# Kernel optimization log

Hardware: AMD Instinct MI355X
Metric: run time of the kernel (lower is better)

## Reference

```python
import jax, jax.numpy as jnp
import numpy as np

N = 20000          # skill_num (nodes)
D = 128            # skill_embed_dim
E = 640000         # edges (avg degree 32)
T = 12             # seq_len
L = 3              # gcn_layers
PRESERVE = 0.1     # residual preserve_ratio


def setup_inputs() -> dict:
    key = jax.random.key(0)
    ks = jax.random.split(key, 8)
    demand_seq_emb = jax.random.normal(ks[0], (N, T, D), jnp.float32)
    supply_seq_emb = jax.random.normal(ks[1], (N, T, D), jnp.float32)
    edge_index = jax.random.randint(ks[2], (2, E), 0, N, dtype=jnp.int32)
    edge_attr = jax.random.uniform(ks[3], (E,), jnp.float32)
    emb_weight = jax.random.normal(ks[4], (N, D), jnp.float32) * 0.02
    fuse_W = jax.random.normal(ks[5], (D, 3 * D), jnp.float32) * (1.0 / np.sqrt(3 * D))
    fuse_b = jnp.zeros((D,), jnp.float32)
    gcn_W = jax.random.normal(ks[6], (L, D, D), jnp.float32) * (1.0 / np.sqrt(D))
    gcn_b = jnp.zeros((L, D), jnp.float32)
    return {
        "demand_seq_emb": demand_seq_emb,
        "supply_seq_emb": supply_seq_emb,
        "l": T, "t_s": 0, "t_e": T,                 # unused by forward (placeholders)
        "edge_index": edge_index,
        "edge_attr": edge_attr,
        "comm": 0, "skill_semantic_embed": 0, "init_emb": 0,  # unused placeholders
        "emb_weight": emb_weight,
        "fuse_W": fuse_W, "fuse_b": fuse_b,
        "gcn_W": gcn_W, "gcn_b": gcn_b,
    }


def _gcn_norm(src, dst, edge_w, n):
    """PyG gcn_norm with self-loops: norm_e = d^-1/2[src] * w_e * d^-1/2[dst]."""
    loop = jnp.arange(n, dtype=src.dtype)
    src2 = jnp.concatenate([src, loop])
    dst2 = jnp.concatenate([dst, loop])
    w2 = jnp.concatenate([edge_w, jnp.ones((n,), edge_w.dtype)])
    deg = jax.ops.segment_sum(w2, dst2, num_segments=n)
    dinv = jnp.where(deg > 0, jax.lax.rsqrt(deg), 0.0)
    norm = dinv[src2] * w2 * dinv[dst2]
    return src2, dst2, norm


def reference(demand_seq_emb, supply_seq_emb, l, t_s, t_e, edge_index, edge_attr,
              comm, skill_semantic_embed, init_emb,
              emb_weight, fuse_W, fuse_b, gcn_W, gcn_b):
    # fuse static embedding with last-step demand/supply sequence embeddings
    seq_last = jnp.concatenate([demand_seq_emb[:, -1, :], supply_seq_emb[:, -1, :]], axis=-1)  # [N,2D]
    fused = jnp.concatenate([emb_weight, seq_last], axis=-1) @ fuse_W.T + fuse_b  # [N,D]

    # edges are generated with all indices < skill_num, so the torch-side
    # `(edge_index < skill_num).all(0)` filter is the identity here.
    src, dst = edge_index[0], edge_index[1]
    src2, dst2, norm = _gcn_norm(src, dst, edge_attr, N)

    temp = fused
    for i in range(L):  # small fixed layer count
        x = temp @ gcn_W[i].T                                   # [N,D] linear (bias added post-agg)
        msg = norm[:, None] * x[src2]                           # gather + scale
        out = jax.ops.segment_sum(msg, dst2, num_segments=N) + gcn_b[i]  # scatter-add
        temp = (1.0 - PRESERVE) * out + PRESERVE * temp         # residual blend
    return temp  # skill_embs [N, D]
```

## Files before the change

### kernel.cpp

```cpp
#include <hip/hip_runtime.h>
#include <hip/hip_fp16.h>

#define NN 20000
#define DD 128
#define EE 640000
#define TSEQ 12
#define CAP 128
#define PADI 32

__device__ __forceinline__ void fma4(float4& acc, float a, const float4& w) {
  acc.x += a * w.x; acc.y += a * w.y; acc.z += a * w.z; acc.w += a * w.w;
}

__device__ __forceinline__ float4 h8_to_f4(uint2 v) {
  union { unsigned u; __half2 h; } a, b;
  a.u = v.x; b.u = v.y;
  float2 fa = __half22float2(a.h);
  float2 fb = __half22float2(b.h);
  return make_float4(fa.x, fa.y, fb.x, fb.y);
}

__device__ __forceinline__ uint2 f4_to_h8(float4 o) {
  union { unsigned u; __half2 h; } a, b;
  a.h = __floats2half2_rn(o.x, o.y);
  b.h = __floats2half2_rn(o.z, o.w);
  uint2 r; r.x = a.u; r.y = b.u;
  return r;
}

__global__ void k_prep(const float* __restrict__ fuse_W,
                       const float* __restrict__ gcn_W,
                       int* __restrict__ cnt_pad,
                       float* __restrict__ fuse_Wt,
                       float* __restrict__ gWt0,
                       __half* __restrict__ gWh) {
  int b = blockIdx.x;
  if (b < 625) {
    int i = b * 256 + threadIdx.x;
    ((int4*)cnt_pad)[i] = make_int4(0, 0, 0, 0);
  } else {
    int i = (b - 625) * 256 + threadIdx.x;
    if (i < 49152) {
      int k = i >> 7, d = i & 127;
      fuse_Wt[i] = fuse_W[d * 384 + k];
    } else if (i < 65536) {
      int j = i - 49152;
      int k = j >> 7, d = j & 127;
      gWt0[j] = gcn_W[d * 128 + k];
    } else if (i < 98304) {
      int j = i - 65536;
      int l = 1 + (j >> 14), jj = j & 16383;
      int k = jj >> 7, d = jj & 127;
      gWh[j] = (__half)gcn_W[l * 16384 + d * 128 + k];
    }
  }
}

#define G_TN 2
#define G_BN 32

template<int KC>
__device__ __forceinline__ void gemm_body(
    float* Ws, int gb,
    const float* a0, int s0, const float* a1, int s1, const float* a2, int s2,
    int nparts, const float* Wt, const float* bias, const float* deg,
    float* outf, uint2* outh)
{
  const int t = threadIdx.x;
  const int dq = t & 15;
  const int ng = t >> 4;
  const int n_base = gb * G_BN + ng * G_TN;

  float4 acc0[G_TN], acc1[G_TN];
  #pragma unroll
  for (int i = 0; i < G_TN; ++i) {
    acc0[i] = make_float4(0.f, 0.f, 0.f, 0.f);
    acc1[i] = make_float4(0.f, 0.f, 0.f, 0.f);
  }

  for (int p = 0; p < nparts; ++p) {
    const float* ap; int as;
    if (p == 0) { ap = a0; as = s0; }
    else if (p == 1) { ap = a1; as = s1; }
    else { ap = a2; as = s2; }
    const float* rp[G_TN];
    #pragma unroll
    for (int i = 0; i < G_TN; ++i) rp[i] = ap + (size_t)(n_base + i) * as;

    for (int c = 0; c < 128 / KC; ++c) {
      const float4* wsrc = (const float4*)(Wt + (p * 128 + c * KC) * 128);
      float4* wdst = (float4*)Ws;
      #pragma unroll
      for (int it = 0; it < KC / 8; ++it) wdst[it * 256 + t] = wsrc[it * 256 + t];
      __syncthreads();

      const int ks = c * KC;
      for (int k = 0; k < KC; k += 4) {
        float4 av[G_TN];
        #pragma unroll
        for (int i = 0; i < G_TN; ++i) av[i] = *(const float4*)(rp[i] + ks + k);
        #pragma unroll
        for (int j = 0; j < 4; ++j) {
          const float4 w0 = *(const float4*)&Ws[(k + j) * 128 + 4 * dq];
          const float4 w1 = *(const float4*)&Ws[(k + j) * 128 + 64 + 4 * dq];
          #pragma unroll
          for (int i = 0; i < G_TN; ++i) {
            float a = (j == 0) ? av[i].x : (j == 1) ? av[i].y : (j == 2) ? av[i].z : av[i].w;
            fma4(acc0[i], a, w0);
            fma4(acc1[i], a, w1);
          }
        }
      }
      __syncthreads();
    }
  }

  float4 b0 = make_float4(0.f,0.f,0.f,0.f), b1 = b0;
  if (bias) {
    b0 = *(const float4*)&bias[4 * dq];
    b1 = *(const float4*)&bias[64 + 4 * dq];
  }
  #pragma unroll
  for (int i = 0; i < G_TN; ++i) {
    int r = n_base + i;
    float4 o0 = make_float4(acc0[i].x + b0.x, acc0[i].y + b0.y,
                            acc0[i].z + b0.z, acc0[i].w + b0.w);
    float4 o1 = make_float4(acc1[i].x + b1.x, acc1[i].y + b1.y,
                            acc1[i].z + b1.z, acc1[i].w + b1.w);
    if (outf) {
      *(float4*)(outf + (size_t)r * DD + 4 * dq) = o0;
      *(float4*)(outf + (size_t)r * DD + 64 + 4 * dq) = o1;
    } else {
      float di = rsqrtf(deg[r]);
      o0.x *= di; o0.y *= di; o0.z *= di; o0.w *= di;
      o1.x *= di; o1.y *= di; o1.z *= di; o1.w *= di;
      outh[(size_t)r * 32 + dq] = f4_to_h8(o0);
      outh[(size_t)r * 32 + 16 + dq] = f4_to_h8(o1);
    }
  }
}

__global__ __launch_bounds__(256, 4) void k_mega(
    const float* __restrict__ emb, const float* __restrict__ demand,
    const float* __restrict__ supply,
    const float* __restrict__ fuse_Wt, const float* __restrict__ fuse_b,
    float* __restrict__ temp0,
    const int* __restrict__ src, const int* __restrict__ dst,
    const float* __restrict__ w,
    int* __restrict__ cnt_pad,
    uint2* __restrict__ csr)
{
  __shared__ float Ws[64 * 128];
  if (blockIdx.x < 625) {
    gemm_body<64>(Ws, blockIdx.x,
                  emb, 128, demand + 11 * 128, TSEQ * 128, supply + 11 * 128, TSEQ * 128,
                  3, fuse_Wt, fuse_b, nullptr, temp0, nullptr);
  } else {
    int e = (blockIdx.x - 625) * 256 + threadIdx.x;
    int s = src[e], d = dst[e];
    float we = w[e];
    int slot = atomicAdd(&cnt_pad[(size_t)d * PADI], 1);
    if (slot < CAP) csr[(size_t)d * CAP + slot] = make_uint2((unsigned)s, __float_as_uint(we));
  }
}

__global__ __launch_bounds__(256, 8) void k_deg(
    const int* __restrict__ cnt_pad, const uint2* __restrict__ csr,
    float* __restrict__ deg)
{
  const int t = threadIdx.x;
  const int lane = t & 7;
  const int ng = t >> 3;
  const int n = blockIdx.x * 32 + ng;
  int m = cnt_pad[(size_t)n * PADI]; if (m > CAP) m = CAP;
  const size_t base = (size_t)n * CAP;
  float s = 0.f;
  for (int j = lane; j < m; j += 8) s += __uint_as_float(csr[base + j].y);
  s += __shfl_xor(s, 1);
  s += __shfl_xor(s, 2);
  s += __shfl_xor(s, 4);
  if (lane == 0) deg[n] = 1.0f + s;
}

__global__ __launch_bounds__(256, 8) void k_gemm_x0(
    const float* __restrict__ temp0, const float* __restrict__ gWt0,
    const float* __restrict__ deg, uint2* __restrict__ outh)
{
  __shared__ float Ws[32 * 128];
  gemm_body<32>(Ws, blockIdx.x, temp0, 128, temp0, 128, temp0, 128,
                1, gWt0, nullptr, deg, nullptr, outh);
}

template<bool NEXT>
__global__ __launch_bounds__(256, 6) void k_agg_fused(
    const uint2* __restrict__ xh, const float* __restrict__ tin,
    const int* __restrict__ cnt_pad, const uint2* __restrict__ csr,
    const float* __restrict__ deg, const float* __restrict__ bias,
    const uint2* __restrict__ Wh,
    float* __restrict__ tout,
    uint2* __restrict__ xh_out)
{
  __shared__ float rows[NEXT ? 8 * 128 : 8];
  __shared__ uint2 Whs[NEXT ? 2048 : 8];

  const int t = threadIdx.x;
  const int dq = t & 31;
  const int nl = t >> 5;
  const int n = blockIdx.x * 8 + nl;

  if constexpr (NEXT) {
    #pragma unroll
    for (int i = 0; i < 8; ++i) Whs[i * 256 + t] = Wh[i * 256 + t];
  }

  const float di = rsqrtf(deg[n]);
  float4 acc = h8_to_f4(xh[(size_t)n * 32 + dq]);

  const size_t base = (size_t)n * CAP;
  int m = cnt_pad[(size_t)n * PADI]; if (m > CAP) m = CAP;
  int j = 0;
  for (; j + 16 <= m; j += 16) {
    uint2 c[16];
    #pragma unroll
    for (int u = 0; u < 16; ++u) c[u] = csr[base + j + u];
    uint2 v[16];
    #pragma unroll
    for (int u = 0; u < 16; ++u) v[u] = xh[(size_t)c[u].x * 32 + dq];
    #pragma unroll
    for (int u = 0; u < 16; ++u) fma4(acc, __uint_as_float(c[u].y), h8_to_f4(v[u]));
  }
  for (; j + 4 <= m; j += 4) {
    uint2 c[4];
    #pragma unroll
    for (int u = 0; u < 4; ++u) c[u] = csr[base + j + u];
    uint2 v[4];
    #pragma unroll
    for (int u = 0; u < 4; ++u) v[u] = xh[(size_t)c[u].x * 32 + dq];
    #pragma unroll
    for (int u = 0; u < 4; ++u) fma4(acc, __uint_as_float(c[u].y), h8_to_f4(v[u]));
  }
  for (; j < m; ++j) {
    uint2 c = csr[base + j];
    fma4(acc, __uint_as_float(c.y), h8_to_f4(xh[(size_t)c.x * 32 + dq]));
  }

  const float4 b4 = *(const float4*)&bias[4 * dq];
  const float4 ti = ((const float4*)tin)[(size_t)n * 32 + dq];
  float4 o;
  o.x = 0.9f * (di * acc.x + b4.x) + 0.1f * ti.x;
  o.y = 0.9f * (di * acc.y + b4.y) + 0.1f * ti.y;
  o.z = 0.9f * (di * acc.z + b4.z) + 0.1f * ti.z;
  o.w = 0.9f * (di * acc.w + b4.w) + 0.1f * ti.w;
  ((float4*)tout)[(size_t)n * 32 + dq] = o;

  if constexpr (NEXT) {
    *(float4*)&rows[nl * 128 + 4 * dq] = o;
    __syncthreads();

    float4 x = make_float4(0.f, 0.f, 0.f, 0.f);
    const float* myrow = &rows[nl * 128];
    #pragma unroll 4
    for (int k = 0; k < 64; ++k) {
      fma4(x, myrow[k], h8_to_f4(Whs[k * 32 + dq]));
    }
    __syncthreads();
    #pragma unroll
    for (int i = 0; i < 8; ++i) Whs[i * 256 + t] = Wh[2048 + i * 256 + t];
    __syncthreads();
    #pragma unroll 4
    for (int k = 0; k < 64; ++k) {
      fma4(x, myrow[64 + k], h8_to_f4(Whs[k * 32 + dq]));
    }
    x.x *= di; x.y *= di; x.z *= di; x.w *= di;
    xh_out[(size_t)n * 32 + dq] = f4_to_h8(x);
  }
}

extern "C" void kernel_launch(void* const* d_in, const int* in_sizes, int n_in,
                              void* d_out, int out_size, void* d_ws, size_t ws_size,
                              hipStream_t stream) {
  const float* demand = (const float*)d_in[0];
  const float* supply = (const float*)d_in[1];
  const int*   eidx   = (const int*)d_in[5];
  const float* eattr  = (const float*)d_in[6];
  const float* emb    = (const float*)d_in[10];
  const float* fuse_W = (const float*)d_in[11];
  const float* fuse_b = (const float*)d_in[12];
  const float* gcn_W  = (const float*)d_in[13];
  const float* gcn_b  = (const float*)d_in[14];
  float* outp = (float*)d_out;

  char* ws = (char*)d_ws;
  size_t o = 0;
  auto alloc = [&](size_t bytes) {
    char* p = ws + o;
    o += (bytes + 255) & ~(size_t)255;
    return p;
  };
  float*  deg     = (float*)alloc((size_t)NN * 4);
  int*    cnt_pad = (int*)alloc((size_t)NN * PADI * 4);
  uint2*  csr     = (uint2*)alloc((size_t)NN * CAP * 8);
  float*  fuse_Wt = (float*)alloc((size_t)384 * 128 * 4);
  float*  gWt0    = (float*)alloc((size_t)128 * 128 * 4);
  __half* gWh     = (__half*)alloc((size_t)2 * 128 * 128 * 2);
  float*  temp0   = (float*)alloc((size_t)NN * DD * 4);
  float*  temp1   = (float*)alloc((size_t)NN * DD * 4);
  uint2*  xh_a    = (uint2*)alloc((size_t)NN * DD * 2);
  uint2*  xh_b    = (uint2*)alloc((size_t)NN * DD * 2);

  const int* srcv = eidx;
  const int* dstv = eidx + EE;

  k_prep<<<1009, 256, 0, stream>>>(fuse_W, gcn_W, cnt_pad, fuse_Wt, gWt0, gWh);

  k_mega<<<3125, 256, 0, stream>>>(emb, demand, supply, fuse_Wt, fuse_b, temp0,
                                   srcv, dstv, eattr, cnt_pad, csr);

  k_deg<<<625, 256, 0, stream>>>(cnt_pad, csr, deg);

  k_gemm_x0<<<625, 256, 0, stream>>>(temp0, gWt0, deg, xh_a);

  const int AB = NN / 8;
  k_agg_fused<true ><<<AB, 256, 0, stream>>>(xh_a, temp0, cnt_pad, csr, deg, gcn_b,
                                             (const uint2*)gWh, temp1, xh_b);
  k_agg_fused<true ><<<AB, 256, 0, stream>>>(xh_b, temp1, cnt_pad, csr, deg, gcn_b + 128,
                                             (const uint2*)(gWh + 16384), temp0, xh_a);
  k_agg_fused<false><<<AB, 256, 0, stream>>>(xh_a, temp0, cnt_pad, csr, deg, gcn_b + 256,
                                             nullptr, outp, nullptr);
}
```

Measured before the change: 406.6 us.

## Fuse first GCN linear into fuse GEMM and prenormalize CSR edge weights

The first GCN layer's linear transform now runs inside the fuse GEMM blocks, using the fused rows staged in shared memory, so the separate k_gemm_x0 pass and its re-read of temp0 go away. Degree normalization moves into a new k_rescale kernel that folds d^-1/2[src]*d^-1/2[dst] into each CSR edge weight once. The aggregation kernels then skip their per-node dinv scaling and read a compact clamped count array instead of the padded counter. The cost is an extra pass over the CSR with random dif lookups, plus more shared memory and register pressure in the mega kernel.

```diff
diff --git a/kernel.cpp b/kernel.cpp
--- a/kernel.cpp
+++ b/kernel.cpp
@@ -56,105 +56,104 @@
   }
 }
 
-#define G_TN 2
-#define G_BN 32
-
-template<int KC>
-__device__ __forceinline__ void gemm_body(
-    float* Ws, int gb,
-    const float* a0, int s0, const float* a1, int s1, const float* a2, int s2,
-    int nparts, const float* Wt, const float* bias, const float* deg,
-    float* outf, uint2* outh)
-{
-  const int t = threadIdx.x;
-  const int dq = t & 15;
-  const int ng = t >> 4;
-  const int n_base = gb * G_BN + ng * G_TN;
-
-  float4 acc0[G_TN], acc1[G_TN];
-  #pragma unroll
-  for (int i = 0; i < G_TN; ++i) {
-    acc0[i] = make_float4(0.f, 0.f, 0.f, 0.f);
-    acc1[i] = make_float4(0.f, 0.f, 0.f, 0.f);
-  }
-
-  for (int p = 0; p < nparts; ++p) {
-    const float* ap; int as;
-    if (p == 0) { ap = a0; as = s0; }
-    else if (p == 1) { ap = a1; as = s1; }
-    else { ap = a2; as = s2; }
-    const float* rp[G_TN];
-    #pragma unroll
-    for (int i = 0; i < G_TN; ++i) rp[i] = ap + (size_t)(n_base + i) * as;
-
-    for (int c = 0; c < 128 / KC; ++c) {
-      const float4* wsrc = (const float4*)(Wt + (p * 128 + c * KC) * 128);
-      float4* wdst = (float4*)Ws;
-      #pragma unroll
-      for (int it = 0; it < KC / 8; ++it) wdst[it * 256 + t] = wsrc[it * 256 + t];
-      __syncthreads();
-
-      const int ks = c * KC;
-      for (int k = 0; k < KC; k += 4) {
-        float4 av[G_TN];
-        #pragma unroll
-        for (int i = 0; i < G_TN; ++i) av[i] = *(const float4*)(rp[i] + ks + k);
-        #pragma unroll
-        for (int j = 0; j < 4; ++j) {
-          const float4 w0 = *(const float4*)&Ws[(k + j) * 128 + 4 * dq];
-          const float4 w1 = *(const float4*)&Ws[(k + j) * 128 + 64 + 4 * dq];
-          #pragma unroll
-          for (int i = 0; i < G_TN; ++i) {
-            float a = (j == 0) ? av[i].x : (j == 1) ? av[i].y : (j == 2) ? av[i].z : av[i].w;
-            fma4(acc0[i], a, w0);
-            fma4(acc1[i], a, w1);
-          }
-        }
-      }
-      __syncthreads();
-    }
-  }
-
-  float4 b0 = make_float4(0.f,0.f,0.f,0.f), b1 = b0;
-  if (bias) {
-    b0 = *(const float4*)&bias[4 * dq];
-    b1 = *(const float4*)&bias[64 + 4 * dq];
-  }
-  #pragma unroll
-  for (int i = 0; i < G_TN; ++i) {
-    int r = n_base + i;
-    float4 o0 = make_float4(acc0[i].x + b0.x, acc0[i].y + b0.y,
-                            acc0[i].z + b0.z, acc0[i].w + b0.w);
-    float4 o1 = make_float4(acc1[i].x + b1.x, acc1[i].y + b1.y,
-                            acc1[i].z + b1.z, acc1[i].w + b1.w);
-    if (outf) {
-      *(float4*)(outf + (size_t)r * DD + 4 * dq) = o0;
-      *(float4*)(outf + (size_t)r * DD + 64 + 4 * dq) = o1;
-    } else {
-      float di = rsqrtf(deg[r]);
-      o0.x *= di; o0.y *= di; o0.z *= di; o0.w *= di;
-      o1.x *= di; o1.y *= di; o1.z *= di; o1.w *= di;
-      outh[(size_t)r * 32 + dq] = f4_to_h8(o0);
-      outh[(size_t)r * 32 + 16 + dq] = f4_to_h8(o1);
-    }
-  }
-}
-
 __global__ __launch_bounds__(256, 4) void k_mega(
     const float* __restrict__ emb, const float* __restrict__ demand,
     const float* __restrict__ supply,
     const float* __restrict__ fuse_Wt, const float* __restrict__ fuse_b,
-    float* __restrict__ temp0,
+    const float* __restrict__ gWt0,
+    float* __restrict__ temp0, uint2* __restrict__ xh0,
     const int* __restrict__ src, const int* __restrict__ dst,
     const float* __restrict__ w,
     int* __restrict__ cnt_pad,
     uint2* __restrict__ csr)
 {
-  __shared__ float Ws[64 * 128];
+  __shared__ float Ws[8448];
   if (blockIdx.x < 625) {
-    gemm_body<64>(Ws, blockIdx.x,
-                  emb, 128, demand + 11 * 128, TSEQ * 128, supply + 11 * 128, TSEQ * 128,
-                  3, fuse_Wt, fuse_b, nullptr, temp0, nullptr);
+    const int t  = threadIdx.x;
+    const int dq = t & 15;
+    const int ng = t >> 4;
+    const int n_base = blockIdx.x * 32 + ng * 2;
+
+    float4 acc0[2], acc1[2];
+    #pragma unroll
+    for (int i = 0; i < 2; ++i) {
+      acc0[i] = make_float4(0.f, 0.f, 0.f, 0.f);
+      acc1[i] = make_float4(0.f, 0.f, 0.f, 0.f);
+    }
+
+    for (int p = 0; p < 3; ++p) {
+      const float* ap; int as;
+      if (p == 0)      { ap = emb;                  as = 128; }
+      else if (p == 1) { ap = demand + 11 * 128;    as = TSEQ * 128; }
+      else             { ap = supply + 11 * 128;    as = TSEQ * 128; }
+      const float* rp0 = ap + (size_t)(n_base + 0) * as;
+      const float* rp1 = ap + (size_t)(n_base + 1) * as;
+
+      for (int c = 0; c < 2; ++c) {
+        const float4* wsrc = (const float4*)(fuse_Wt + (p * 128 + c * 64) * 128);
+        float4* wdst = (float4*)Ws;
+        #pragma unroll
+        for (int it = 0; it < 8; ++it) wdst[it * 256 + t] = wsrc[it * 256 + t];
+        __syncthreads();
+
+        const int ks = c * 64;
+        for (int k = 0; k < 64; k += 4) {
+          float4 av0 = *(const float4*)(rp0 + ks + k);
+          float4 av1 = *(const float4*)(rp1 + ks + k);
+          #pragma unroll
+          for (int j = 0; j < 4; ++j) {
+            const float4 w0 = *(const float4*)&Ws[(k + j) * 128 + 4 * dq];
+            const float4 w1 = *(const float4*)&Ws[(k + j) * 128 + 64 + 4 * dq];
+            float a0 = (j == 0) ? av0.x : (j == 1) ? av0.y : (j == 2) ? av0.z : av0.w;
+            float a1 = (j == 0) ? av1.x : (j == 1) ? av1.y : (j == 2) ? av1.z : av1.w;
+            fma4(acc0[0], a0, w0); fma4(acc1[0], a0, w1);
+            fma4(acc0[1], a1, w0); fma4(acc1[1], a1, w1);
+          }
+        }
+        __syncthreads();
+      }
+    }
+
+    const float4 b0 = *(const float4*)&fuse_b[4 * dq];
+    const float4 b1 = *(const float4*)&fuse_b[64 + 4 * dq];
+    #pragma unroll
+    for (int i = 0; i < 2; ++i) {
+      const int r  = n_base + i;
+      const int lr = ng * 2 + i;
+      float4 o0 = make_float4(acc0[i].x + b0.x, acc0[i].y + b0.y,
+                              acc0[i].z + b0.z, acc0[i].w + b0.w);
+      float4 o1 = make_float4(acc1[i].x + b1.x, acc1[i].y + b1.y,
+                              acc1[i].z + b1.z, acc1[i].w + b1.w);
+      *(float4*)(temp0 + (size_t)r * DD + 4 * dq)      = o0;
+      *(float4*)(temp0 + (size_t)r * DD + 64 + 4 * dq) = o1;
+      *(float4*)&Ws[lr * 132 + 4 * dq]      = o0;
+      *(float4*)&Ws[lr * 132 + 64 + 4 * dq] = o1;
+    }
+
+    float4 x00 = make_float4(0.f,0.f,0.f,0.f), x01 = x00, x10 = x00, x11 = x00;
+    const int lr0 = ng * 2, lr1 = ng * 2 + 1;
+    float* WsW = Ws + 4224;
+    for (int c2 = 0; c2 < 4; ++c2) {
+      const float4* wsrc = (const float4*)(gWt0 + c2 * 32 * 128);
+      float4* wdst = (float4*)WsW;
+      #pragma unroll
+      for (int it = 0; it < 4; ++it) wdst[it * 256 + t] = wsrc[it * 256 + t];
+      __syncthreads();
+      const int ks = c2 * 32;
+      for (int k = 0; k < 32; ++k) {
+        const float a0 = Ws[lr0 * 132 + ks + k];
+        const float a1 = Ws[lr1 * 132 + ks + k];
+        const float4 w0 = *(const float4*)&WsW[k * 128 + 4 * dq];
+        const float4 w1 = *(const float4*)&WsW[k * 128 + 64 + 4 * dq];
+        fma4(x00, a0, w0); fma4(x01, a0, w1);
+        fma4(x10, a1, w0); fma4(x11, a1, w1);
+      }
+      __syncthreads();
+    }
+    xh0[(size_t)(n_base + 0) * 32 + dq]      = f4_to_h8(x00);
+    xh0[(size_t)(n_base + 0) * 32 + 16 + dq] = f4_to_h8(x01);
+    xh0[(size_t)(n_base + 1) * 32 + dq]      = f4_to_h8(x10);
+    xh0[(size_t)(n_base + 1) * 32 + 16 + dq] = f4_to_h8(x11);
   } else {
     int e = (blockIdx.x - 625) * 256 + threadIdx.x;
     int s = src[e], d = dst[e];
@@ -166,7 +165,7 @@
 
 __global__ __launch_bounds__(256, 8) void k_deg(
     const int* __restrict__ cnt_pad, const uint2* __restrict__ csr,
-    float* __restrict__ deg)
+    float* __restrict__ dif, int* __restrict__ cntc)
 {
   const int t = threadIdx.x;
   const int lane = t & 7;
@@ -179,23 +178,32 @@
   s += __shfl_xor(s, 1);
   s += __shfl_xor(s, 2);
   s += __shfl_xor(s, 4);
-  if (lane == 0) deg[n] = 1.0f + s;
-}
-
-__global__ __launch_bounds__(256, 8) void k_gemm_x0(
-    const float* __restrict__ temp0, const float* __restrict__ gWt0,
-    const float* __restrict__ deg, uint2* __restrict__ outh)
+  if (lane == 0) { dif[n] = rsqrtf(1.0f + s); cntc[n] = m; }
+}
+
+__global__ __launch_bounds__(256, 8) void k_rescale(
+    const int* __restrict__ cntc, const float* __restrict__ dif,
+    uint2* __restrict__ csr)
 {
-  __shared__ float Ws[32 * 128];
-  gemm_body<32>(Ws, blockIdx.x, temp0, 128, temp0, 128, temp0, 128,
-                1, gWt0, nullptr, deg, nullptr, outh);
+  const int t = threadIdx.x;
+  const int lane = t & 31;
+  const int nl = t >> 5;
+  const int n = blockIdx.x * 8 + nl;
+  const int m = cntc[n];
+  const float dn = dif[n];
+  const size_t base = (size_t)n * CAP;
+  for (int j = lane; j < m; j += 32) {
+    uint2 c = csr[base + j];
+    float wp = __uint_as_float(c.y) * dn * dif[c.x];
+    ((unsigned*)csr)[(base + j) * 2 + 1] = __float_as_uint(wp);
+  }
 }
 
 template<bool NEXT>
 __global__ __launch_bounds__(256, 6) void k_agg_fused(
     const uint2* __restrict__ xh, const float* __restrict__ tin,
-    const int* __restrict__ cnt_pad, const uint2* __restrict__ csr,
-    const float* __restrict__ deg, const float* __restrict__ bias,
+    const int* __restrict__ cntc, const uint2* __restrict__ csr,
+    const float* __restrict__ dif, const float* __restrict__ bias,
     const uint2* __restrict__ Wh,
     float* __restrict__ tout,
     uint2* __restrict__ xh_out)
@@ -213,11 +221,13 @@
     for (int i = 0; i < 8; ++i) Whs[i * 256 + t] = Wh[i * 256 + t];
   }
 
-  const float di = rsqrtf(deg[n]);
-  float4 acc = h8_to_f4(xh[(size_t)n * 32 + dq]);
+  const float dfn = dif[n];
+  const float d2 = dfn * dfn;
+  float4 sv = h8_to_f4(xh[(size_t)n * 32 + dq]);
+  float4 acc = make_float4(d2 * sv.x, d2 * sv.y, d2 * sv.z, d2 * sv.w);
 
   const size_t base = (size_t)n * CAP;
-  int m = cnt_pad[(size_t)n * PADI]; if (m > CAP) m = CAP;
+  const int m = cntc[n];
   int j = 0;
   for (; j + 16 <= m; j += 16) {
     uint2 c[16];
@@ -247,10 +257,10 @@
   const float4 b4 = *(const float4*)&bias[4 * dq];
   const float4 ti = ((const float4*)tin)[(size_t)n * 32 + dq];
   float4 o;
-  o.x = 0.9f * (di * acc.x + b4.x) + 0.1f * ti.x;
-  o.y = 0.9f * (di * acc.y + b4.y) + 0.1f * ti.y;
-  o.z = 0.9f * (di * acc.z + b4.z) + 0.1f * ti.z;
-  o.w = 0.9f * (di * acc.w + b4.w) + 0.1f * ti.w;
+  o.x = 0.9f * (acc.x + b4.x) + 0.1f * ti.x;
+  o.y = 0.9f * (acc.y + b4.y) + 0.1f * ti.y;
+  o.z = 0.9f * (acc.z + b4.z) + 0.1f * ti.z;
+  o.w = 0.9f * (acc.w + b4.w) + 0.1f * ti.w;
   ((float4*)tout)[(size_t)n * 32 + dq] = o;
 
   if constexpr (NEXT) {
@@ -271,7 +281,6 @@
     for (int k = 0; k < 64; ++k) {
       fma4(x, myrow[64 + k], h8_to_f4(Whs[k * 32 + dq]));
     }
-    x.x *= di; x.y *= di; x.z *= di; x.w *= di;
     xh_out[(size_t)n * 32 + dq] = f4_to_h8(x);
   }
 }
@@ -297,7 +306,8 @@
     o += (bytes + 255) & ~(size_t)255;
     return p;
   };
-  float*  deg     = (float*)alloc((size_t)NN * 4);
+  float*  dif     = (float*)alloc((size_t)NN * 4);
+  int*    cntc    = (int*)alloc((size_t)NN * 4);
   int*    cnt_pad = (int*)alloc((size_t)NN * PADI * 4);
   uint2*  csr     = (uint2*)alloc((size_t)NN * CAP * 8);
   float*  fuse_Wt = (float*)alloc((size_t)384 * 128 * 4);
@@ -313,18 +323,18 @@
 
   k_prep<<<1009, 256, 0, stream>>>(fuse_W, gcn_W, cnt_pad, fuse_Wt, gWt0, gWh);
 
-  k_mega<<<3125, 256, 0, stream>>>(emb, demand, supply, fuse_Wt, fuse_b, temp0,
-                                   srcv, dstv, eattr, cnt_pad, csr);
-
-  k_deg<<<625, 256, 0, stream>>>(cnt_pad, csr, deg);
-
-  k_gemm_x0<<<625, 256, 0, stream>>>(temp0, gWt0, deg, xh_a);
+  k_mega<<<3125, 256, 0, stream>>>(emb, demand, supply, fuse_Wt, fuse_b, gWt0,
+                                   temp0, xh_a, srcv, dstv, eattr, cnt_pad, csr);
+
+  k_deg<<<625, 256, 0, stream>>>(cnt_pad, csr, dif, cntc);
+
+  k_rescale<<<2500, 256, 0, stream>>>(cntc, dif, csr);
 
   const int AB = NN / 8;
-  k_agg_fused<true ><<<AB, 256, 0, stream>>>(xh_a, temp0, cnt_pad, csr, deg, gcn_b,
+  k_agg_fused<true ><<<AB, 256, 0, stream>>>(xh_a, temp0, cntc, csr, dif, gcn_b,
                                              (const uint2*)gWh, temp1, xh_b);
-  k_agg_fused<true ><<<AB, 256, 0, stream>>>(xh_b, temp1, cnt_pad, csr, deg, gcn_b + 128,
+  k_agg_fused<true ><<<AB, 256, 0, stream>>>(xh_b, temp1, cntc, csr, dif, gcn_b + 128,
                                              (const uint2*)(gWh + 16384), temp0, xh_a);
-  k_agg_fused<false><<<AB, 256, 0, stream>>>(xh_a, temp0, cnt_pad, csr, deg, gcn_b + 256,
+  k_agg_fused<false><<<AB, 256, 0, stream>>>(xh_a, temp0, cntc, csr, dif, gcn_b + 256,
                                              nullptr, outp, nullptr);
 }
```

Result: slower. 415.1 us (+2.1%).

## Pack CSR entries to 32-bit with fp16 weights and fuse degree into x0 GEMM

Applied to the files above, without the earlier changes.

Each CSR slot now stores the source index in the upper 16 bits and an fp16 edge weight in the lower 16 bits, halving the CSR bytes read in the three aggregation passes. The degree kernel is merged into the first GCN linear GEMM, which also writes a precomputed rsqrt degree and a compact clamped count array, removing one launch and the padded-count reads. Packing node indices into 16 bits only holds because N is 20000, below 65536, and fp16 weights lose precision compared with the fp32 originals.

```diff
diff --git a/kernel.cpp b/kernel.cpp
--- a/kernel.cpp
+++ b/kernel.cpp
@@ -26,6 +26,10 @@
   b.h = __floats2half2_rn(o.z, o.w);
   uint2 r; r.x = a.u; r.y = b.u;
   return r;
+}
+
+__device__ __forceinline__ float slot_w(unsigned c) {
+  return __half2float(__ushort_as_half((unsigned short)(c & 0xffffu)));
 }
 
 __global__ void k_prep(const float* __restrict__ fuse_W,
@@ -56,87 +60,67 @@
   }
 }
 
-#define G_TN 2
-#define G_BN 32
-
-template<int KC>
-__device__ __forceinline__ void gemm_body(
+__device__ __forceinline__ void fuse_gemm_body(
     float* Ws, int gb,
-    const float* a0, int s0, const float* a1, int s1, const float* a2, int s2,
-    int nparts, const float* Wt, const float* bias, const float* deg,
-    float* outf, uint2* outh)
+    const float* a0, const float* a1, const float* a2,
+    const float* Wt, const float* bias, float* outf)
 {
   const int t = threadIdx.x;
   const int dq = t & 15;
   const int ng = t >> 4;
-  const int n_base = gb * G_BN + ng * G_TN;
-
-  float4 acc0[G_TN], acc1[G_TN];
+  const int n_base = gb * 32 + ng * 2;
+
+  float4 acc0[2], acc1[2];
   #pragma unroll
-  for (int i = 0; i < G_TN; ++i) {
+  for (int i = 0; i < 2; ++i) {
     acc0[i] = make_float4(0.f, 0.f, 0.f, 0.f);
     acc1[i] = make_float4(0.f, 0.f, 0.f, 0.f);
   }
 
-  for (int p = 0; p < nparts; ++p) {
+  for (int p = 0; p < 3; ++p) {
     const float* ap; int as;
-    if (p == 0) { ap = a0; as = s0; }
-    else if (p == 1) { ap = a1; as = s1; }
-    else { ap = a2; as = s2; }
-    const float* rp[G_TN];
-    #pragma unroll
-    for (int i = 0; i < G_TN; ++i) rp[i] = ap + (size_t)(n_base + i) * as;
-
-    for (int c = 0; c < 128 / KC; ++c) {
-      const float4* wsrc = (const float4*)(Wt + (p * 128 + c * KC) * 128);
+    if (p == 0)      { ap = a0; as = 128; }
+    else if (p == 1) { ap = a1; as = TSEQ * 128; }
+    else             { ap = a2; as = TSEQ * 128; }
+    const float* rp0 = ap + (size_t)(n_base + 0) * as;
+    const float* rp1 = ap + (size_t)(n_base + 1) * as;
+
+    for (int c = 0; c < 2; ++c) {
+      const float4* wsrc = (const float4*)(Wt + (p * 128 + c * 64) * 128);
       float4* wdst = (float4*)Ws;
       #pragma unroll
-      for (int it = 0; it < KC / 8; ++it) wdst[it * 256 + t] = wsrc[it * 256 + t];
+      for (int it = 0; it < 8; ++it) wdst[it * 256 + t] = wsrc[it * 256 + t];
       __syncthreads();
 
-      const int ks = c * KC;
-      for (int k = 0; k < KC; k += 4) {
-        float4 av[G_TN];
-        #pragma unroll
-        for (int i = 0; i < G_TN; ++i) av[i] = *(const float4*)(rp[i] + ks + k);
+      const int ks = c * 64;
+      for (int k = 0; k < 64; k += 4) {
+        float4 av0 = *(const float4*)(rp0 + ks + k);
+        float4 av1 = *(const float4*)(rp1 + ks + k);
         #pragma unroll
         for (int j = 0; j < 4; ++j) {
           const float4 w0 = *(const float4*)&Ws[(k + j) * 128 + 4 * dq];
           const float4 w1 = *(const float4*)&Ws[(k + j) * 128 + 64 + 4 * dq];
-          #pragma unroll
-          for (int i = 0; i < G_TN; ++i) {
-            float a = (j == 0) ? av[i].x : (j == 1) ? av[i].y : (j == 2) ? av[i].z : av[i].w;
-            fma4(acc0[i], a, w0);
-            fma4(acc1[i], a, w1);
-          }
+          float a0v = (j == 0) ? av0.x : (j == 1) ? av0.y : (j == 2) ? av0.z : av0.w;
+          float a1v = (j == 0) ? av1.x : (j == 1) ? av1.y : (j == 2) ? av1.z : av1.w;
+          fma4(acc0[0], a0v, w0); fma4(acc1[0], a0v, w1);
+          fma4(acc0[1], a1v, w0); fma4(acc1[1], a1v, w1);
         }
       }
       __syncthreads();
     }
   }
 
-  float4 b0 = make_float4(0.f,0.f,0.f,0.f), b1 = b0;
-  if (bias) {
-    b0 = *(const float4*)&bias[4 * dq];
-    b1 = *(const float4*)&bias[64 + 4 * dq];
-  }
+  const float4 b0 = *(const float4*)&bias[4 * dq];
+  const float4 b1 = *(const float4*)&bias[64 + 4 * dq];
   #pragma unroll
-  for (int i = 0; i < G_TN; ++i) {
-    int r = n_base + i;
+  for (int i = 0; i < 2; ++i) {
+    const int r = n_base + i;
     float4 o0 = make_float4(acc0[i].x + b0.x, acc0[i].y + b0.y,
                             acc0[i].z + b0.z, acc0[i].w + b0.w);
     float4 o1 = make_float4(acc1[i].x + b1.x, acc1[i].y + b1.y,
                             acc1[i].z + b1.z, acc1[i].w + b1.w);
-    if (outf) {
-      *(float4*)(outf + (size_t)r * DD + 4 * dq) = o0;
-      *(float4*)(outf + (size_t)r * DD + 64 + 4 * dq) = o1;
-    } else {
-      float di = rsqrtf(deg[r]);
-      o0.x *= di; o0.y *= di; o0.z *= di; o0.w *= di;
-      o1.x *= di; o1.y *= di; o1.z *= di; o1.w *= di;
-      outh[(size_t)r * 32 + dq] = f4_to_h8(o0);
-      outh[(size_t)r * 32 + 16 + dq] = f4_to_h8(o1);
-    }
+    *(float4*)(outf + (size_t)r * DD + 4 * dq)      = o0;
+    *(float4*)(outf + (size_t)r * DD + 64 + 4 * dq) = o1;
   }
 }
 
@@ -148,54 +132,101 @@
     const int* __restrict__ src, const int* __restrict__ dst,
     const float* __restrict__ w,
     int* __restrict__ cnt_pad,
-    uint2* __restrict__ csr)
+    unsigned* __restrict__ csr)
 {
   __shared__ float Ws[64 * 128];
   if (blockIdx.x < 625) {
-    gemm_body<64>(Ws, blockIdx.x,
-                  emb, 128, demand + 11 * 128, TSEQ * 128, supply + 11 * 128, TSEQ * 128,
-                  3, fuse_Wt, fuse_b, nullptr, temp0, nullptr);
+    fuse_gemm_body(Ws, blockIdx.x,
+                   emb, demand + 11 * 128, supply + 11 * 128,
+                   fuse_Wt, fuse_b, temp0);
   } else {
     int e = (blockIdx.x - 625) * 256 + threadIdx.x;
     int s = src[e], d = dst[e];
     float we = w[e];
     int slot = atomicAdd(&cnt_pad[(size_t)d * PADI], 1);
-    if (slot < CAP) csr[(size_t)d * CAP + slot] = make_uint2((unsigned)s, __float_as_uint(we));
-  }
-}
-
-__global__ __launch_bounds__(256, 8) void k_deg(
-    const int* __restrict__ cnt_pad, const uint2* __restrict__ csr,
-    float* __restrict__ deg)
-{
-  const int t = threadIdx.x;
-  const int lane = t & 7;
-  const int ng = t >> 3;
-  const int n = blockIdx.x * 32 + ng;
-  int m = cnt_pad[(size_t)n * PADI]; if (m > CAP) m = CAP;
-  const size_t base = (size_t)n * CAP;
-  float s = 0.f;
-  for (int j = lane; j < m; j += 8) s += __uint_as_float(csr[base + j].y);
-  s += __shfl_xor(s, 1);
-  s += __shfl_xor(s, 2);
-  s += __shfl_xor(s, 4);
-  if (lane == 0) deg[n] = 1.0f + s;
-}
-
-__global__ __launch_bounds__(256, 8) void k_gemm_x0(
+    if (slot < CAP)
+      csr[(size_t)d * CAP + slot] =
+          ((unsigned)s << 16) | (unsigned)__half_as_ushort(__float2half_rn(we));
+  }
+}
+
+__global__ __launch_bounds__(256, 8) void k_x0deg(
     const float* __restrict__ temp0, const float* __restrict__ gWt0,
-    const float* __restrict__ deg, uint2* __restrict__ outh)
+    const int* __restrict__ cnt_pad, const unsigned* __restrict__ csr,
+    float* __restrict__ dif, int* __restrict__ cntc,
+    uint2* __restrict__ outh)
 {
   __shared__ float Ws[32 * 128];
-  gemm_body<32>(Ws, blockIdx.x, temp0, 128, temp0, 128, temp0, 128,
-                1, gWt0, nullptr, deg, nullptr, outh);
+  __shared__ float difs[32];
+
+  const int t = threadIdx.x;
+
+  {
+    const int lane = t & 7;
+    const int ng8 = t >> 3;
+    const int n = blockIdx.x * 32 + ng8;
+    int m = cnt_pad[(size_t)n * PADI]; if (m > CAP) m = CAP;
+    const size_t base = (size_t)n * CAP;
+    float s = 0.f;
+    for (int j = lane; j < m; j += 8) s += slot_w(csr[base + j]);
+    s += __shfl_xor(s, 1);
+    s += __shfl_xor(s, 2);
+    s += __shfl_xor(s, 4);
+    if (lane == 0) {
+      float df = rsqrtf(1.0f + s);
+      dif[n] = df; cntc[n] = m; difs[ng8] = df;
+    }
+  }
+  __syncthreads();
+
+  const int dq = t & 15;
+  const int ng = t >> 4;
+  const int n_base = blockIdx.x * 32 + ng * 2;
+  const float* rp0 = temp0 + (size_t)(n_base + 0) * DD;
+  const float* rp1 = temp0 + (size_t)(n_base + 1) * DD;
+
+  float4 a00 = make_float4(0.f,0.f,0.f,0.f), a01 = a00, a10 = a00, a11 = a00;
+  for (int c = 0; c < 4; ++c) {
+    const float4* wsrc = (const float4*)(gWt0 + c * 32 * 128);
+    float4* wdst = (float4*)Ws;
+    #pragma unroll
+    for (int it = 0; it < 4; ++it) wdst[it * 256 + t] = wsrc[it * 256 + t];
+    __syncthreads();
+
+    const int ks = c * 32;
+    for (int k = 0; k < 32; k += 4) {
+      float4 av0 = *(const float4*)(rp0 + ks + k);
+      float4 av1 = *(const float4*)(rp1 + ks + k);
+      #pragma unroll
+      for (int j = 0; j < 4; ++j) {
+        const float4 w0 = *(const float4*)&Ws[(k + j) * 128 + 4 * dq];
+        const float4 w1 = *(const float4*)&Ws[(k + j) * 128 + 64 + 4 * dq];
+        float a0v = (j == 0) ? av0.x : (j == 1) ? av0.y : (j == 2) ? av0.z : av0.w;
+        float a1v = (j == 0) ? av1.x : (j == 1) ? av1.y : (j == 2) ? av1.z : av1.w;
+        fma4(a00, a0v, w0); fma4(a01, a0v, w1);
+        fma4(a10, a1v, w0); fma4(a11, a1v, w1);
+      }
+    }
+    __syncthreads();
+  }
+
+  const float d0 = difs[ng * 2 + 0];
+  const float d1 = difs[ng * 2 + 1];
+  a00.x *= d0; a00.y *= d0; a00.z *= d0; a00.w *= d0;
+  a01.x *= d0; a01.y *= d0; a01.z *= d0; a01.w *= d0;
+  a10.x *= d1; a10.y *= d1; a10.z *= d1; a10.w *= d1;
+  a11.x *= d1; a11.y *= d1; a11.z *= d1; a11.w *= d1;
+  outh[(size_t)(n_base + 0) * 32 + dq]      = f4_to_h8(a00);
+  outh[(size_t)(n_base + 0) * 32 + 16 + dq] = f4_to_h8(a01);
+  outh[(size_t)(n_base + 1) * 32 + dq]      = f4_to_h8(a10);
+  outh[(size_t)(n_base + 1) * 32 + 16 + dq] = f4_to_h8(a11);
 }
 
 template<bool NEXT>
 __global__ __launch_bounds__(256, 6) void k_agg_fused(
     const uint2* __restrict__ xh, const float* __restrict__ tin,
-    const int* __restrict__ cnt_pad, const uint2* __restrict__ csr,
-    const float* __restrict__ deg, const float* __restrict__ bias,
+    const int* __restrict__ cntc, const unsigned* __restrict__ csr,
+    const float* __restrict__ dif, const float* __restrict__ bias,
     const uint2* __restrict__ Wh,
     float* __restrict__ tout,
     uint2* __restrict__ xh_out)
@@ -213,35 +244,35 @@
     for (int i = 0; i < 8; ++i) Whs[i * 256 + t] = Wh[i * 256 + t];
   }
 
-  const float di = rsqrtf(deg[n]);
+  const float di = rsqrtf(1.0f) * dif[n];
   float4 acc = h8_to_f4(xh[(size_t)n * 32 + dq]);
 
   const size_t base = (size_t)n * CAP;
-  int m = cnt_pad[(size_t)n * PADI]; if (m > CAP) m = CAP;
+  const int m = cntc[n];
   int j = 0;
   for (; j + 16 <= m; j += 16) {
-    uint2 c[16];
+    unsigned c[16];
     #pragma unroll
     for (int u = 0; u < 16; ++u) c[u] = csr[base + j + u];
     uint2 v[16];
     #pragma unroll
-    for (int u = 0; u < 16; ++u) v[u] = xh[(size_t)c[u].x * 32 + dq];
-    #pragma unroll
-    for (int u = 0; u < 16; ++u) fma4(acc, __uint_as_float(c[u].y), h8_to_f4(v[u]));
+    for (int u = 0; u < 16; ++u) v[u] = xh[(size_t)(c[u] >> 16) * 32 + dq];
+    #pragma unroll
+    for (int u = 0; u < 16; ++u) fma4(acc, slot_w(c[u]), h8_to_f4(v[u]));
   }
   for (; j + 4 <= m; j += 4) {
-    uint2 c[4];
+    unsigned c[4];
     #pragma unroll
     for (int u = 0; u < 4; ++u) c[u] = csr[base + j + u];
     uint2 v[4];
     #pragma unroll
-    for (int u = 0; u < 4; ++u) v[u] = xh[(size_t)c[u].x * 32 + dq];
-    #pragma unroll
-    for (int u = 0; u < 4; ++u) fma4(acc, __uint_as_float(c[u].y), h8_to_f4(v[u]));
+    for (int u = 0; u < 4; ++u) v[u] = xh[(size_t)(c[u] >> 16) * 32 + dq];
+    #pragma unroll
+    for (int u = 0; u < 4; ++u) fma4(acc, slot_w(c[u]), h8_to_f4(v[u]));
   }
   for (; j < m; ++j) {
-    uint2 c = csr[base + j];
-    fma4(acc, __uint_as_float(c.y), h8_to_f4(xh[(size_t)c.x * 32 + dq]));
+    unsigned c = csr[base + j];
+    fma4(acc, slot_w(c), h8_to_f4(xh[(size_t)(c >> 16) * 32 + dq]));
   }
 
   const float4 b4 = *(const float4*)&bias[4 * dq];
@@ -297,16 +328,17 @@
     o += (bytes + 255) & ~(size_t)255;
     return p;
   };
-  float*  deg     = (float*)alloc((size_t)NN * 4);
-  int*    cnt_pad = (int*)alloc((size_t)NN * PADI * 4);
-  uint2*  csr     = (uint2*)alloc((size_t)NN * CAP * 8);
-  float*  fuse_Wt = (float*)alloc((size_t)384 * 128 * 4);
-  float*  gWt0    = (float*)alloc((size_t)128 * 128 * 4);
-  __half* gWh     = (__half*)alloc((size_t)2 * 128 * 128 * 2);
-  float*  temp0   = (float*)alloc((size_t)NN * DD * 4);
-  float*  temp1   = (float*)alloc((size_t)NN * DD * 4);
-  uint2*  xh_a    = (uint2*)alloc((size_t)NN * DD * 2);
-  uint2*  xh_b    = (uint2*)alloc((size_t)NN * DD * 2);
+  float*    dif     = (float*)alloc((size_t)NN * 4);
+  int*      cntc    = (int*)alloc((size_t)NN * 4);
+  int*      cnt_pad = (int*)alloc((size_t)NN * PADI * 4);
+  unsigned* csr     = (unsigned*)alloc((size_t)NN * CAP * 4);
+  float*    fuse_Wt = (float*)alloc((size_t)384 * 128 * 4);
+  float*    gWt0    = (float*)alloc((size_t)128 * 128 * 4);
+  __half*   gWh     = (__half*)alloc((size_t)2 * 128 * 128 * 2);
+  float*    temp0   = (float*)alloc((size_t)NN * DD * 4);
+  float*    temp1   = (float*)alloc((size_t)NN * DD * 4);
+  uint2*    xh_a    = (uint2*)alloc((size_t)NN * DD * 2);
+  uint2*    xh_b    = (uint2*)alloc((size_t)NN * DD * 2);
 
   const int* srcv = eidx;
   const int* dstv = eidx + EE;
@@ -316,15 +348,13 @@
   k_mega<<<3125, 256, 0, stream>>>(emb, demand, supply, fuse_Wt, fuse_b, temp0,
                                    srcv, dstv, eattr, cnt_pad, csr);
 
-  k_deg<<<625, 256, 0, stream>>>(cnt_pad, csr, deg);
-
-  k_gemm_x0<<<625, 256, 0, stream>>>(temp0, gWt0, deg, xh_a);
+  k_x0deg<<<625, 256, 0, stream>>>(temp0, gWt0, cnt_pad, csr, dif, cntc, xh_a);
 
   const int AB = NN / 8;
-  k_agg_fused<true ><<<AB, 256, 0, stream>>>(xh_a, temp0, cnt_pad, csr, deg, gcn_b,
+  k_agg_fused<true ><<<AB, 256, 0, stream>>>(xh_a, temp0, cntc, csr, dif, gcn_b,
                                              (const uint2*)gWh, temp1, xh_b);
-  k_agg_fused<true ><<<AB, 256, 0, stream>>>(xh_b, temp1, cnt_pad, csr, deg, gcn_b + 128,
+  k_agg_fused<true ><<<AB, 256, 0, stream>>>(xh_b, temp1, cntc, csr, dif, gcn_b + 128,
                                              (const uint2*)(gWh + 16384), temp0, xh_a);
-  k_agg_fused<false><<<AB, 256, 0, stream>>>(xh_a, temp0, cnt_pad, csr, deg, gcn_b + 256,
+  k_agg_fused<false><<<AB, 256, 0, stream>>>(xh_a, temp0, cntc, csr, dif, gcn_b + 256,
                                              nullptr, outp, nullptr);
 }
```

New measurement: 394.3 us. 1.03x faster.
